# Kernel optimization log

Hardware: AMD Instinct MI355X
Metric: run time of the kernel (lower is better)

Reference implementation:

```python
import jax, jax.numpy as jnp
import numpy as np

L = 1024       # qlen
B = 2          # batch
D = 1024       # hidden_size
NH = 16        # heads
DH = 64        # d_head
NL = 4         # num_hidden_layers
MLEN = 1024    # memory length
KLEN = MLEN + L


def setup_inputs() -> dict:
    key = jax.random.key(0)
    ks = jax.random.split(key, 10)
    s = 0.02
    # causal mask: key position j is masked (True) if j > mlen + i
    attn_mask = (jnp.arange(KLEN)[None, :] > (MLEN + jnp.arange(L))[:, None])[:, :, None]
    return {
        "mems": jax.random.normal(ks[0], (NL + 1, MLEN, B, D), jnp.float32),
        "raw_embeddings": jax.random.normal(ks[1], (L, B, D), jnp.float32),
        "attention_mask": attn_mask,
        "r_w_bias": jax.random.normal(ks[2], (NH, DH), jnp.float32) * s,
        "r_r_bias": jax.random.normal(ks[3], (NH, DH), jnp.float32) * s,
        "qkv_w": jax.random.normal(ks[4], (NL, D, 3 * NH * DH), jnp.float32) * s,
        "r_w": jax.random.normal(ks[5], (NL, D, NH * DH), jnp.float32) * s,
        "o_w": jax.random.normal(ks[6], (NL, NH * DH, D), jnp.float32) * s,
        "ln1_g": jnp.ones((NL, D), jnp.float32),
        "ln1_b": jnp.zeros((NL, D), jnp.float32),
        "ff_w1": jax.random.normal(ks[7], (NL, D, D), jnp.float32) * s,
        "ff_b1": jnp.zeros((NL, D), jnp.float32),
        "ff_w2": jax.random.normal(ks[8], (NL, D, D), jnp.float32) * s,
        "ff_b2": jnp.zeros((NL, D), jnp.float32),
        "ln2_g": jnp.ones((NL, D), jnp.float32),
        "ln2_b": jnp.zeros((NL, D), jnp.float32),
    }


def _layernorm(x, g, b, eps=1e-5):
    m = jnp.mean(x, axis=-1, keepdims=True)
    v = jnp.var(x, axis=-1, keepdims=True)
    return (x - m) / jnp.sqrt(v + eps) * g + b


def _rel_shift(x):
    # x: (qlen, rlen, b, n) -> XL relative shift via pad/reshape trick
    q, r, b, n = x.shape
    xp = jnp.pad(x, ((0, 0), (1, 0), (0, 0), (0, 0)))     # (q, r+1, b, n)
    xp = xp.reshape(r + 1, q, b, n)                        # flat reinterpret
    return xp[1:].reshape(q, r, b, n)


def _forward(mems, raw_embeddings, attention_mask, r_w_bias, r_r_bias, qkv_w, r_w,
             o_w, ln1_g, ln1_b, ff_w1, ff_b1, ff_w2, ff_b2, ln2_g, ln2_b):
    qlen, bsz, d = raw_embeddings.shape
    mlen = mems.shape[1]
    klen = mlen + qlen
    nh, dh = r_w_bias.shape
    scale = 1.0 / (dh ** 0.5)

    # sinusoidal relative positional embedding: pos_seq = klen-1 ... 0
    pos_seq = jnp.arange(klen - 1, -1, -1, dtype=raw_embeddings.dtype)
    inv_freq = 1.0 / (10000.0 ** (jnp.arange(0, d, 2, dtype=jnp.float32) / d))
    sinusoid = pos_seq[:, None] * inv_freq[None, :]
    pos_emb = jnp.concatenate([jnp.sin(sinusoid), jnp.cos(sinusoid)], axis=-1)  # (klen, D)

    mask = attention_mask[:, :, :, None]  # (L, 2L, 1, 1)
    core = raw_embeddings
    hids = [core]
    n_layers = qkv_w.shape[0]
    for i in range(n_layers):
        cat = jnp.concatenate([mems[i], core], axis=0)          # (klen, b, D)
        w_heads = cat @ qkv_w[i]                                # (klen, b, 3D)
        q, k, v = jnp.split(w_heads, 3, axis=-1)
        q = q[-qlen:]
        q = q.reshape(qlen, bsz, nh, dh)
        k = k.reshape(klen, bsz, nh, dh)
        v = v.reshape(klen, bsz, nh, dh)
        r_head_k = (pos_emb @ r_w[i]).reshape(klen, nh, dh)     # (rlen, n, d)

        AC = jnp.einsum('ibnd,jbnd->ijbn', q + r_w_bias, k)
        BD = _rel_shift(jnp.einsum('ibnd,jnd->ijbn', q + r_r_bias, r_head_k))
        score = (AC + BD) * scale                               # (q, k, b, n)
        score = jnp.where(mask, -jnp.inf, score)
        prob = jax.nn.softmax(score, axis=1)
        attn_vec = jnp.einsum('ijbn,jbnd->ibnd', prob, v).reshape(qlen, bsz, nh * dh)
        attn_out = attn_vec @ o_w[i]
        core = _layernorm(core + attn_out, ln1_g[i], ln1_b[i])  # post-lnorm

        ff = jnp.maximum(core @ ff_w1[i] + ff_b1[i], 0.0) @ ff_w2[i] + ff_b2[i]
        core = _layernorm(core + ff, ln2_g[i], ln2_b[i])
        hids.append(core)

    new_mems = jax.lax.stop_gradient(jnp.stack(hids, axis=0))   # xl_grad=False -> detach
    return core, new_mems


def reference(mems, raw_embeddings, attention_mask, r_w_bias, r_r_bias, qkv_w, r_w,
              o_w, ln1_g, ln1_b, ff_w1, ff_b1, ff_w2, ff_b2, ln2_g, ln2_b):
    return _forward(mems, raw_embeddings, attention_mask, r_w_bias, r_r_bias, qkv_w,
                    r_w, o_w, ln1_g, ln1_b, ff_w1, ff_b1, ff_w2, ff_b2, ln2_g, ln2_b)
```

## Files before the change

### kernel.cpp

```cpp
#include <hip/hip_runtime.h>
#include <hip/hip_bf16.h>

#define QLEN 1024
#define BSZ 2
#define DIM 1024
#define NH 16
#define DH 64
#define NL 4
#define MLEN 1024
#define KLEN 2048
#define QROWS (QLEN*BSZ)
#define CATROWS (KLEN*BSZ)
#define N3 (3*NH*DH)

typedef __hip_bfloat16 bf16;
typedef short bf16x8_t __attribute__((ext_vector_type(8)));
typedef float f32x4_t __attribute__((ext_vector_type(4)));

__device__ __forceinline__ float b2f(bf16 h) { return __bfloat162float(h); }
__device__ __forceinline__ bf16 f2b(float f) { return __float2bfloat16(f); }
__device__ __forceinline__ short f2bs(float f) {
  bf16 h = f2b(f);
  return *reinterpret_cast<short*>(&h);
}

__device__ __forceinline__ float loadf(const void* p, size_t i, int isb) {
  return isb ? b2f(((const bf16*)p)[i]) : ((const float*)p)[i];
}
__device__ __forceinline__ void storef(void* p, size_t i, float v, int isb) {
  if (isb) ((bf16*)p)[i] = f2b(v);
  else     ((float*)p)[i] = v;
}

__device__ __forceinline__ bf16x8_t load_bf8(const bf16* p) {
  union { uint4 u; bf16x8_t v; } x;
  x.u = *reinterpret_cast<const uint4*>(p);
  return x.v;
}

__device__ __forceinline__ void gld_lds16(const bf16* g, bf16* l) {
  __builtin_amdgcn_global_load_lds(
      (const __attribute__((address_space(1))) void*)g,
      (__attribute__((address_space(3))) void*)l, 16, 0, 0);
}

__global__ void probe_kernel(const void* g, int* flag) {
  *flag = (((const unsigned int*)g)[0] == 0x3F803F80u) ? 1 : 0;
}

__global__ void pos_emb_kernel(bf16* __restrict__ pe) {
  int idx = blockIdx.x * 256 + threadIdx.x;
  int j = idx >> 10;
  int c = idx & 1023;
  int fi = (c < 512) ? c : (c - 512);
  float inv = expf(-((float)(2 * fi) * (1.0f / 1024.0f)) * 9.210340371976184f);
  float pos = (float)(KLEN - 1 - j);
  float a = pos * inv;
  float v = (c < 512) ? sinf(a) : cosf(a);
  pe[idx] = f2b(v);
}

__global__ void init_kernel(const void* __restrict__ raw, float* __restrict__ core,
                            void* __restrict__ out, const int* __restrict__ flag) {
  const int isb = *flag;
  int idx = blockIdx.x * 256 + threadIdx.x;
  float v = loadf(raw, idx, isb);
  core[idx] = v;
  storef(out, (size_t)QROWS * DIM + idx, v, isb);
}

__global__ void concat_kernel(const void* __restrict__ mems, size_t memsOff,
                              const float* __restrict__ core,
                              bf16* __restrict__ cat, const int* __restrict__ flag) {
  const int isb = *flag;
  int idx = blockIdx.x * 256 + threadIdx.x;
  const int memElems = MLEN * BSZ * DIM;
  if (idx < memElems) cat[idx] = f2b(loadf(mems, memsOff + idx, isb));
  else                cat[idx] = f2b(core[idx - memElems]);
}

__global__ void transpose5_kernel(const void* __restrict__ qkvw, const void* __restrict__ rw,
                                  const void* __restrict__ ow, const void* __restrict__ ffw1,
                                  const void* __restrict__ ffw2,
                                  bf16* __restrict__ qkvT, bf16* __restrict__ rwT,
                                  bf16* __restrict__ owT, bf16* __restrict__ f1T,
                                  bf16* __restrict__ f2T,
                                  int layer, const int* __restrict__ flag) {
  const int isb = *flag;
  __shared__ float tile[32][33];
  const int n0 = blockIdx.x * 32;
  const int k0 = blockIdx.y * 32;
  const int tx = threadIdx.x & 31;
  const int ty = threadIdx.x >> 5;
  auto doT = [&](const void* W, size_t wOff, bf16* WT, int K, int N) {
    __syncthreads();
#pragma unroll
    for (int r = 0; r < 32; r += 8)
      tile[ty + r][tx] = loadf(W, wOff + (size_t)(k0 + ty + r) * N + n0 + tx, isb);
    __syncthreads();
#pragma unroll
    for (int r = 0; r < 32; r += 8)
      WT[(size_t)(n0 + ty + r) * K + k0 + tx] = f2b(tile[tx][ty + r]);
  };
  doT(qkvw, (size_t)layer * DIM * N3, qkvT, DIM, N3);
  if (n0 < DIM) {
    const size_t o = (size_t)layer * DIM * DIM;
    doT(rw,   o, rwT, DIM, DIM);
    doT(ow,   o, owT, DIM, DIM);
    doT(ffw1, o, f1T, DIM, DIM);
    doT(ffw2, o, f2T, DIM, DIM);
  }
}

template <int EPI, int BM>
__launch_bounds__(256, 2)
__global__ void mgemm_kernel(const bf16* __restrict__ A, const bf16* __restrict__ Bt,
                             float* __restrict__ Cf, bf16* __restrict__ Ch,
                             bf16* __restrict__ Vt,
                             const void* __restrict__ bias, size_t biasOff,
                             int M, int N, int K, const int* __restrict__ flag) {
  const int isb = *flag;
  constexpr int BN = (BM == 128) ? 128 : 64;
  __shared__ bf16 As[BM * 32];
  __shared__ bf16 Bs[BN * 32];
  const int t = threadIdx.x;
  const int wave = t >> 6;
  const int lane = t & 63;
  const int g  = lane >> 4;
  const int lo = lane & 15;
  const int rowA = blockIdx.y * BM;
  const int rowB = blockIdx.x * BN;

  if constexpr (BM == 128) {
    const int wr = wave >> 1, wc = wave & 1;
    const int srow = wave * 32 + (lane >> 2);
    const int scol = (lane & 3) * 8;
    const bf16* gA = A  + (size_t)(rowA + srow) * K + scol;
    const bf16* gB = Bt + (size_t)(rowB + srow) * K + scol;
    bf16* lA = As + wave * 32 * 32;
    bf16* lB = Bs + wave * 32 * 32;

    f32x4_t acc[4][4];
#pragma unroll
    for (int m = 0; m < 4; ++m)
#pragma unroll
      for (int n = 0; n < 4; ++n) acc[m][n] = (f32x4_t){0.f, 0.f, 0.f, 0.f};

    for (int k0 = 0; k0 < K; k0 += 32) {
      gld_lds16(gA + k0, lA);
      gld_lds16(gA + (size_t)16 * K + k0, lA + 16 * 32);
      gld_lds16(gB + k0, lB);
      gld_lds16(gB + (size_t)16 * K + k0, lB + 16 * 32);
      __syncthreads();
      bf16x8_t af[4], bfr[4];
#pragma unroll
      for (int m = 0; m < 4; ++m)
        af[m] = *reinterpret_cast<const bf16x8_t*>(As + (wr * 64 + m * 16 + lo) * 32 + g * 8);
#pragma unroll
      for (int n = 0; n < 4; ++n)
        bfr[n] = *reinterpret_cast<const bf16x8_t*>(Bs + (wc * 64 + n * 16 + lo) * 32 + g * 8);
#pragma unroll
      for (int m = 0; m < 4; ++m)
#pragma unroll
        for (int n = 0; n < 4; ++n)
          acc[m][n] = __builtin_amdgcn_mfma_f32_16x16x32_bf16(af[m], bfr[n], acc[m][n], 0, 0, 0);
      __syncthreads();
    }

#pragma unroll
    for (int m = 0; m < 4; ++m) {
#pragma unroll
      for (int n = 0; n < 4; ++n) {
        const int col = rowB + wc * 64 + n * 16 + lo;
        float bv = 0.f;
        if constexpr (EPI >= 2 && EPI <= 3) bv = loadf(bias, biasOff + col, isb);
#pragma unroll
        for (int r = 0; r < 4; ++r) {
          const int row = rowA + wr * 64 + m * 16 + g * 4 + r;
          float v = acc[m][n][r];
          const size_t o = (size_t)row * N + col;
          if constexpr (EPI == 0)      Cf[o] = v;
          else if constexpr (EPI == 1) Ch[o] = f2b(v);
          else if constexpr (EPI == 2) { v += bv; Ch[o] = f2b(fmaxf(v, 0.f)); }
          else if constexpr (EPI == 3) { v += bv; Cf[o] = v; }
          else {
            if (col < 2 * DIM) Ch[o] = f2b(v);
            else Vt[((size_t)(row & 1) * DIM + (col - 2 * DIM)) * KLEN + (row >> 1)] = f2b(v);
          }
        }
      }
    }
  } else {
    const int srow = t >> 2;
    const int scol = (t & 3) * 8;
    const bf16* gA = A  + (size_t)(rowA + srow) * K + scol;
    const bf16* gB = Bt + (size_t)(rowB + srow) * K + scol;
    bf16* lA = As + wave * 16 * 32;
    bf16* lB = Bs + wave * 16 * 32;

    f32x4_t acc[4];
#pragma unroll
    for (int n = 0; n < 4; ++n) acc[n] = (f32x4_t){0.f, 0.f, 0.f, 0.f};

    for (int k0 = 0; k0 < K; k0 += 32) {
      gld_lds16(gA + k0, lA);
      gld_lds16(gB + k0, lB);
      __syncthreads();
      bf16x8_t af = *reinterpret_cast<const bf16x8_t*>(As + (wave * 16 + lo) * 32 + g * 8);
      bf16x8_t bfr[4];
#pragma unroll
      for (int n = 0; n < 4; ++n)
        bfr[n] = *reinterpret_cast<const bf16x8_t*>(Bs + (n * 16 + lo) * 32 + g * 8);
#pragma unroll
      for (int n = 0; n < 4; ++n)
        acc[n] = __builtin_amdgcn_mfma_f32_16x16x32_bf16(af, bfr[n], acc[n], 0, 0, 0);
      __syncthreads();
    }

#pragma unroll
    for (int n = 0; n < 4; ++n) {
      const int col = rowB + n * 16 + lo;
      float bv = 0.f;
      if constexpr (EPI >= 2) bv = loadf(bias, biasOff + col, isb);
#pragma unroll
      for (int r = 0; r < 4; ++r) {
        const int row = rowA + wave * 16 + g * 4 + r;
        float v = acc[n][r];
        const size_t o = (size_t)row * N + col;
        if constexpr (EPI == 0)      Cf[o] = v;
        else if constexpr (EPI == 1) Ch[o] = f2b(v);
        else if constexpr (EPI == 2) { v += bv; Ch[o] = f2b(fmaxf(v, 0.f)); }
        else if constexpr (EPI == 3) { v += bv; Cf[o] = v; }
      }
    }
  }
}

#define PSTR 56

__launch_bounds__(256, 4)
__global__ void attn_mfma_kernel(const bf16* __restrict__ wh, const bf16* __restrict__ vT,
                                 const bf16* __restrict__ rk,
                                 const void* __restrict__ rwb, const void* __restrict__ rrb,
                                 float* __restrict__ pO, float* __restrict__ pm,
                                 float* __restrict__ pl, const int* __restrict__ flag) {
  const int isb = *flag;
  const int bid = blockIdx.x;
  const int x  = bid & 7;
  const int j  = bid >> 3;
  const int head = x * 4 + (j & 3);
  const int b = head >> 4;
  const int n = head & 15;
  const int jj = j >> 2;
  const int kh = jj >> 4;
  const int s  = jj & 15;
  const int qb = (s < 8) ? s : 23 - s;
  const int qbase = qb * 64;
  const int T = 17 + qb;
  const int jstart = kh * T * 32;
  const int jlast  = jstart + (T - 1) * 32;
  const int t = threadIdx.x;
  const int wid = t >> 6;
  const int lane = t & 63;
  const int lo = lane & 15;
  const int g  = lane >> 4;
  const int i0 = qbase + wid * 16;

  __shared__ bf16 Kls[2][32 * 64];
  __shared__ bf16 Vtls[2][64 * 32];
  __shared__ bf16 Rls[128 * 64];
  __shared__ short PlsAll[4][16 * PSTR];
  short* Pl = PlsAll[wid];

  const int srow = t >> 3;
  const int kchunk = (t & 7) ^ (srow & 7);
  const size_t rowStride = (size_t)BSZ * N3;
  const bf16* gK  = wh + ((size_t)srow * BSZ + b) * N3 + DIM + n * DH + kchunk * 8;
  const bf16* gVt = vT + ((size_t)b * DIM + n * DH + (t >> 2)) * KLEN
                       + (((t & 3) ^ ((t >> 3) & 3)) << 3);

  auto stageR = [&](int s0) {
    int r = s0 + (t >> 3);
    int rc = (r < KLEN) ? r : (KLEN - 1);
    const bf16* src = rk + (size_t)rc * DIM + n * DH + ((t & 7) ^ ((t >> 3) & 7)) * 8;
    gld_lds16(src, &Rls[(size_t)(s0 & 127) * 64 + (size_t)wid * 512]);
  };

  bf16x8_t qw[2], qr[2];
  {
    const bf16* qrow = wh + ((size_t)(MLEN + i0 + lo) * BSZ + b) * N3 + n * DH;
#pragma unroll
    for (int c = 0; c < 2; ++c) {
      int d0 = c * 32 + g * 8;
#pragma unroll
      for (int jj2 = 0; jj2 < 8; ++jj2) {
        float qv = b2f(qrow[d0 + jj2]);
        qw[c][jj2] = f2bs(qv + loadf(rwb, n * DH + d0 + jj2, isb));
        qr[c][jj2] = f2bs(qv + loadf(rrb, n * DH + d0 + jj2, isb));
      }
    }
  }

  f32x4_t O[4];
  float mrow[4], lrow[4];
#pragma unroll
  for (int d = 0; d < 4; ++d) { O[d] = (f32x4_t){0.f, 0.f, 0.f, 0.f}; }
#pragma unroll
  for (int r = 0; r < 4; ++r) { mrow[r] = -INFINITY; lrow[r] = 0.f; }

  const float SCL = 0.125f * 1.44269504088896f;

  gld_lds16(gK + (size_t)jstart * rowStride, &Kls[0][wid * 512]);
  gld_lds16(gVt + jstart, &Vtls[0][wid * 512]);
  stageR(MLEN - 64 - qbase + jstart);
  stageR(MLEN - 32 - qbase + jstart);
  stageR(MLEN - qbase + jstart);
  __syncthreads();

  int bi = 0;
  for (int j0 = jstart; j0 <= jlast; j0 += 32) {
    if (j0 < jlast) {
      gld_lds16(gK + (size_t)(j0 + 32) * rowStride, &Kls[bi ^ 1][wid * 512]);
      gld_lds16(gVt + j0 + 32, &Vtls[bi ^ 1][wid * 512]);
      stageR(MLEN + 32 + j0 - qbase);
    }
    const bf16* Kl  = Kls[bi];
    const bf16* Vtl = Vtls[bi];

    f32x4_t s2[2];
    s2[0] = (f32x4_t){0.f, 0.f, 0.f, 0.f};
    s2[1] = (f32x4_t){0.f, 0.f, 0.f, 0.f};
#pragma unroll
    for (int c = 0; c < 2; ++c) {
#pragma unroll
      for (int tt = 0; tt < 2; ++tt) {
        const int row = tt * 16 + lo;
        const bf16* kp = Kl + row * 64 + (((c * 4 + g) ^ (row & 7)) << 3);
        s2[tt] = __builtin_amdgcn_mfma_f32_16x16x32_bf16(qw[c], load_bf8(kp), s2[tt], 0, 0, 0);
      }
    }
    const int u0 = MLEN - 1 + j0 - i0 - 15;
    f32x4_t dacc[3];
    dacc[0] = (f32x4_t){0.f, 0.f, 0.f, 0.f};
    dacc[1] = (f32x4_t){0.f, 0.f, 0.f, 0.f};
    dacc[2] = (f32x4_t){0.f, 0.f, 0.f, 0.f};
#pragma unroll
    for (int c = 0; c < 2; ++c) {
#pragma unroll
      for (int tt = 0; tt < 3; ++tt) {
        const int sr = (u0 + tt * 16 + lo) & 127;
        const bf16* rp = Rls + sr * 64 + (((c * 4 + g) ^ (lo & 7)) << 3);
        dacc[tt] = __builtin_amdgcn_mfma_f32_16x16x32_bf16(qr[c], load_bf8(rp), dacc[tt], 0, 0, 0);
      }
    }

    float sv[2][4];
#pragma unroll
    for (int r = 0; r < 4; ++r) {
      const int ri = g * 4 + r;
      const int srcl = g * 16 + ((lo + 15 - ri) & 15);
      float a0 = __shfl(dacc[0][r], srcl);
      float a1 = __shfl(dacc[1][r], srcl);
      float a2 = __shfl(dacc[2][r], srcl);
      const bool hi = lo > ri;
      float d0 = hi ? a1 : a0;
      float d1 = hi ? a2 : a1;
      bool v0 = (kh == 0) || ((j0 + lo)      <= (MLEN + i0 + ri));
      bool v1 = (kh == 0) || ((j0 + lo + 16) <= (MLEN + i0 + ri));
      sv[0][r] = v0 ? (s2[0][r] + d0) * SCL : -INFINITY;
      sv[1][r] = v1 ? (s2[1][r] + d1) * SCL : -INFINITY;
    }

    float alpha[4];
#pragma unroll
    for (int r = 0; r < 4; ++r) {
      float v = fmaxf(sv[0][r], sv[1][r]);
      v = fmaxf(v, __shfl_xor(v, 1));
      v = fmaxf(v, __shfl_xor(v, 2));
      v = fmaxf(v, __shfl_xor(v, 4));
      v = fmaxf(v, __shfl_xor(v, 8));
      float mn = fmaxf(mrow[r], v);
      alpha[r] = exp2f(mrow[r] - mn);
      mrow[r] = mn;
    }
    float ps[2][4];
#pragma unroll
    for (int f2 = 0; f2 < 2; ++f2)
#pragma unroll
      for (int r = 0; r < 4; ++r)
        ps[f2][r] = exp2f(sv[f2][r] - mrow[r]);
#pragma unroll
    for (int r = 0; r < 4; ++r) {
      float v = ps[0][r] + ps[1][r];
      v += __shfl_xor(v, 1);
      v += __shfl_xor(v, 2);
      v += __shfl_xor(v, 4);
      v += __shfl_xor(v, 8);
      lrow[r] = lrow[r] * alpha[r] + v;
    }
#pragma unroll
    for (int d = 0; d < 4; ++d)
#pragma unroll
      for (int r = 0; r < 4; ++r)
        O[d][r] *= alpha[r];

#pragma unroll
    for (int f2 = 0; f2 < 2; ++f2)
#pragma unroll
      for (int r = 0; r < 4; ++r)
        Pl[(g * 4 + r) * PSTR + lo + 16 * f2] = f2bs(ps[f2][r]);
    __builtin_amdgcn_wave_barrier();
    bf16x8_t pf = *reinterpret_cast<const bf16x8_t*>(&Pl[lo * PSTR + g * 8]);

#pragma unroll
    for (int dt = 0; dt < 4; ++dt) {
      const int vrow = dt * 16 + lo;
      bf16x8_t vf = load_bf8(Vtl + vrow * 32 + ((g ^ ((lo >> 1) & 3)) << 3));
      O[dt] = __builtin_amdgcn_mfma_f32_16x16x32_bf16(pf, vf, O[dt], 0, 0, 0);
    }

    __syncthreads();
    bi ^= 1;
  }

#pragma unroll
  for (int dt = 0; dt < 4; ++dt)
#pragma unroll
    for (int r = 0; r < 4; ++r) {
      const int ri = g * 4 + r;
      pO[((size_t)kh * QROWS + (size_t)(i0 + ri) * BSZ + b) * DIM
         + n * DH + dt * 16 + lo] = O[dt][r];
    }
  if (lo == 0) {
#pragma unroll
    for (int r = 0; r < 4; ++r) {
      const int ri = g * 4 + r;
      const size_t sidx = (((size_t)kh * BSZ + b) * NH + n) * QLEN + (i0 + ri);
      pm[sidx] = mrow[r];
      pl[sidx] = lrow[r];
    }
  }
}

__launch_bounds__(256)
__global__ void attn_merge_kernel(const float* __restrict__ pO, const float* __restrict__ pm,
                                  const float* __restrict__ pl, bf16* __restrict__ av) {
  const int row = blockIdx.x;
  const int i = row >> 1;
  const int b = row & 1;
  const int t = threadIdx.x;
  const size_t SH = (size_t)BSZ * NH * QLEN;
#pragma unroll
  for (int u = 0; u < 4; ++u) {
    const int d = t + u * 256;
    const int n = d >> 6;
    const size_t sidx = ((size_t)b * NH + n) * QLEN + i;
    const float m0 = pm[sidx], m1 = pm[SH + sidx];
    const float l0 = pl[sidx], l1 = pl[SH + sidx];
    const float m = fmaxf(m0, m1);
    const float c0 = exp2f(m0 - m), c1 = exp2f(m1 - m);
    const float O0 = pO[(size_t)row * DIM + d];
    const float O1 = pO[((size_t)QROWS + row) * DIM + d];
    av[(size_t)row * DIM + d] = f2b((O0 * c0 + O1 * c1) / (l0 * c0 + l1 * c1));
  }
}

template <bool WRITE_HID>
__launch_bounds__(256)
__global__ void resid_ln_kernel(const float* __restrict__ base, const float* __restrict__ add,
                                const void* __restrict__ g, size_t gOff,
                                const void* __restrict__ bta, size_t btaOff,
                                float* __restrict__ core_f, bf16* __restrict__ core_h,
                                void* __restrict__ out, size_t hidOff,
                                const int* __restrict__ flag) {
  const int isb = *flag;
  const int row = blockIdx.x;
  const int t = threadIdx.x;
  __shared__ float red[256];
  __shared__ float red2[256];
  float x[4];
  float s = 0.f, sq = 0.f;
#pragma unroll
  for (int u = 0; u < 4; ++u) {
    int idx = t + u * 256;
    float v = base[(size_t)row * DIM + idx] + add[(size_t)row * DIM + idx];
    x[u] = v; s += v; sq += v * v;
  }
  red[t] = s; red2[t] = sq; __syncthreads();
#pragma unroll
  for (int s2 = 128; s2 > 0; s2 >>= 1) {
    if (t < s2) { red[t] += red[t + s2]; red2[t] += red2[t + s2]; }
    __syncthreads();
  }
  const float mean = red[0] * (1.0f / DIM);
  const float var  = red2[0] * (1.0f / DIM) - mean * mean;
  const float rstd = rsqrtf(var + 1e-5f);
#pragma unroll
  for (int u = 0; u < 4; ++u) {
    int idx = t + u * 256;
    float y = (x[u] - mean) * rstd * loadf(g, gOff + idx, isb) + loadf(bta, btaOff + idx, isb);
    core_f[(size_t)row * DIM + idx] = y;
    core_h[(size_t)row * DIM + idx] = f2b(y);
    if (WRITE_HID) storef(out, hidOff + (size_t)row * DIM + idx, y, isb);
  }
}

__global__ void copy_out_kernel(const float* __restrict__ src, void* __restrict__ out,
                                const int* __restrict__ flag) {
  const int isb = *flag;
  int idx = blockIdx.x * 256 + threadIdx.x;
  storef(out, idx, src[idx], isb);
}

extern "C" void kernel_launch(void* const* d_in, const int* in_sizes, int n_in,
                              void* d_out, int out_size, void* d_ws, size_t ws_size,
                              hipStream_t stream) {
  const void* mems = d_in[0];
  const void* raw  = d_in[1];
  const void* rwb  = d_in[3];
  const void* rrb  = d_in[4];
  const void* qkvw = d_in[5];
  const void* rw   = d_in[6];
  const void* ow   = d_in[7];
  const void* ln1g = d_in[8];
  const void* ln1b = d_in[9];
  const void* ffw1 = d_in[10];
  const void* ffb1 = d_in[11];
  const void* ffw2 = d_in[12];
  const void* ffb2 = d_in[13];
  const void* ln2g = d_in[14];
  const void* ln2b = d_in[15];

  char* w = (char*)d_ws;
  size_t off = 0;
  auto alloc = [&](size_t bytes) -> void* {
    void* p = w + off;
    off += (bytes + 255) & ~(size_t)255;
    return p;
  };
  int*   flag    = (int*)alloc(4);
  bf16*  pos_emb = (bf16*)alloc((size_t)KLEN * DIM * 2);
  bf16*  wh      = (bf16*)alloc((size_t)CATROWS * N3 * 2);
  bf16*  cat     = (bf16*)alloc((size_t)CATROWS * DIM * 2);
  bf16*  rk      = (bf16*)alloc((size_t)KLEN * DIM * 2);
  float* core_f  = (float*)alloc((size_t)QROWS * DIM * 4);
  bf16*  vT      = (bf16*)alloc((size_t)2 * DIM * KLEN * 2);
  float* pO      = (float*)alloc((size_t)2 * QROWS * DIM * 4);
  float* pm      = (float*)alloc((size_t)2 * BSZ * NH * QLEN * 4);
  float* pl      = (float*)alloc((size_t)2 * BSZ * NH * QLEN * 4);
  bf16*  qkvT    = (bf16*)alloc((size_t)N3 * DIM * 2);
  bf16*  rwT     = (bf16*)alloc((size_t)DIM * DIM * 2);
  bf16*  owT     = (bf16*)alloc((size_t)DIM * DIM * 2);
  bf16*  f1T     = (bf16*)alloc((size_t)DIM * DIM * 2);
  bf16*  f2T     = (bf16*)alloc((size_t)DIM * DIM * 2);
  float* buf1   = (float*)wh;
  bf16*  buf2   = (bf16*)((char*)wh + (size_t)8 * 1024 * 1024);
  bf16*  avec   = cat;
  bf16*  core_h = (bf16*)((char*)cat + (size_t)4 * 1024 * 1024);
  (void)ws_size; (void)in_sizes; (void)n_in; (void)out_size;

  const size_t HID = (size_t)QROWS * DIM;

  probe_kernel<<<1, 1, 0, stream>>>(ln1g, flag);
  pos_emb_kernel<<<KLEN * DIM / 256, 256, 0, stream>>>(pos_emb);
  init_kernel<<<QROWS * DIM / 256, 256, 0, stream>>>(raw, core_f, d_out, flag);

  for (int i = 0; i < NL; ++i) {
    const size_t memsOff = (size_t)i * MLEN * BSZ * DIM;
    transpose5_kernel<<<dim3(96, 32), 256, 0, stream>>>(
        qkvw, rw, ow, ffw1, ffw2, qkvT, rwT, owT, f1T, f2T, i, flag);
    concat_kernel<<<CATROWS * DIM / 256, 256, 0, stream>>>(mems, memsOff, core_f, cat, flag);
    mgemm_kernel<4, 128><<<dim3(N3 / 128, CATROWS / 128), 256, 0, stream>>>(
        cat, qkvT, nullptr, wh, vT, nullptr, 0, CATROWS, N3, DIM, flag);
    mgemm_kernel<1, 64><<<dim3(DIM / 64, KLEN / 64), 256, 0, stream>>>(
        pos_emb, rwT, nullptr, rk, nullptr, nullptr, 0, KLEN, DIM, DIM, flag);
    attn_mfma_kernel<<<1024, 256, 0, stream>>>(wh, vT, rk, rwb, rrb, pO, pm, pl, flag);
    attn_merge_kernel<<<QROWS, 256, 0, stream>>>(pO, pm, pl, avec);
    mgemm_kernel<0, 64><<<dim3(DIM / 64, QROWS / 64), 256, 0, stream>>>(
        avec, owT, buf1, nullptr, nullptr, nullptr, 0, QROWS, DIM, DIM, flag);
    resid_ln_kernel<false><<<QROWS, 256, 0, stream>>>(
        core_f, buf1, ln1g, (size_t)i * DIM, ln1b, (size_t)i * DIM,
        core_f, core_h, nullptr, 0, flag);
    mgemm_kernel<2, 64><<<dim3(DIM / 64, QROWS / 64), 256, 0, stream>>>(
        core_h, f1T, nullptr, buf2, nullptr, ffb1, (size_t)i * DIM, QROWS, DIM, DIM, flag);
    mgemm_kernel<3, 64><<<dim3(DIM / 64, QROWS / 64), 256, 0, stream>>>(
        buf2, f2T, buf1, nullptr, nullptr, ffb2, (size_t)i * DIM, QROWS, DIM, DIM, flag);
    resid_ln_kernel<true><<<QROWS, 256, 0, stream>>>(
        core_f, buf1, ln2g, (size_t)i * DIM, ln2b, (size_t)i * DIM,
        core_f, core_h, d_out, HID * (size_t)(i + 2), flag);
  }
  copy_out_kernel<<<QROWS * DIM / 256, 256, 0, stream>>>(core_f, d_out, flag);
}
```

Measured before the change: 1.248 ms.

## Double-buffer 64-tile GEMM with K=64 stages and XOR swizzle; vectorize attn merge

Splits the 64x64 GEMM path into a separate kernel that loads K=64 slices into double-buffered LDS. The next tile is prefetched while the current one is computed, and an XOR swizzle avoids LDS bank conflicts. This halves the number of barriers per K step and hides global-load latency. The attention merge kernel now has each thread handle four contiguous elements, using float4 loads, one reciprocal and a packed bf16 store. The cost is more LDS per block (32KB), which may reduce occupancy, and relies on load_bf8 existing in the hidden code.

```diff
diff --git a/kernel.cpp b/kernel.cpp
--- a/kernel.cpp
+++ b/kernel.cpp
@@ -112,7 +112,7 @@
   }
 }
 
-template <int EPI, int BM>
+template <int EPI>
 __launch_bounds__(256, 2)
 __global__ void mgemm_kernel(const bf16* __restrict__ A, const bf16* __restrict__ Bt,
                              float* __restrict__ Cf, bf16* __restrict__ Ch,
@@ -120,118 +120,144 @@
                              const void* __restrict__ bias, size_t biasOff,
                              int M, int N, int K, const int* __restrict__ flag) {
   const int isb = *flag;
-  constexpr int BN = (BM == 128) ? 128 : 64;
-  __shared__ bf16 As[BM * 32];
-  __shared__ bf16 Bs[BN * 32];
+  __shared__ bf16 As[128 * 32];
+  __shared__ bf16 Bs[128 * 32];
   const int t = threadIdx.x;
   const int wave = t >> 6;
   const int lane = t & 63;
   const int g  = lane >> 4;
   const int lo = lane & 15;
-  const int rowA = blockIdx.y * BM;
-  const int rowB = blockIdx.x * BN;
-
-  if constexpr (BM == 128) {
-    const int wr = wave >> 1, wc = wave & 1;
-    const int srow = wave * 32 + (lane >> 2);
-    const int scol = (lane & 3) * 8;
-    const bf16* gA = A  + (size_t)(rowA + srow) * K + scol;
-    const bf16* gB = Bt + (size_t)(rowB + srow) * K + scol;
-    bf16* lA = As + wave * 32 * 32;
-    bf16* lB = Bs + wave * 32 * 32;
-
-    f32x4_t acc[4][4];
+  const int wr = wave >> 1, wc = wave & 1;
+  const int rowA = blockIdx.y * 128;
+  const int rowB = blockIdx.x * 128;
+
+  const int srow = wave * 32 + (lane >> 2);
+  const int scol = (lane & 3) * 8;
+  const bf16* gA = A  + (size_t)(rowA + srow) * K + scol;
+  const bf16* gB = Bt + (size_t)(rowB + srow) * K + scol;
+  bf16* lA = As + wave * 32 * 32;
+  bf16* lB = Bs + wave * 32 * 32;
+
+  f32x4_t acc[4][4];
+#pragma unroll
+  for (int m = 0; m < 4; ++m)
+#pragma unroll
+    for (int n = 0; n < 4; ++n) acc[m][n] = (f32x4_t){0.f, 0.f, 0.f, 0.f};
+
+  for (int k0 = 0; k0 < K; k0 += 32) {
+    gld_lds16(gA + k0, lA);
+    gld_lds16(gA + (size_t)16 * K + k0, lA + 16 * 32);
+    gld_lds16(gB + k0, lB);
+    gld_lds16(gB + (size_t)16 * K + k0, lB + 16 * 32);
+    __syncthreads();
+    bf16x8_t af[4], bfr[4];
 #pragma unroll
     for (int m = 0; m < 4; ++m)
-#pragma unroll
-      for (int n = 0; n < 4; ++n) acc[m][n] = (f32x4_t){0.f, 0.f, 0.f, 0.f};
-
-    for (int k0 = 0; k0 < K; k0 += 32) {
-      gld_lds16(gA + k0, lA);
-      gld_lds16(gA + (size_t)16 * K + k0, lA + 16 * 32);
-      gld_lds16(gB + k0, lB);
-      gld_lds16(gB + (size_t)16 * K + k0, lB + 16 * 32);
-      __syncthreads();
-      bf16x8_t af[4], bfr[4];
-#pragma unroll
-      for (int m = 0; m < 4; ++m)
-        af[m] = *reinterpret_cast<const bf16x8_t*>(As + (wr * 64 + m * 16 + lo) * 32 + g * 8);
+      af[m] = *reinterpret_cast<const bf16x8_t*>(As + (wr * 64 + m * 16 + lo) * 32 + g * 8);
+#pragma unroll
+    for (int n = 0; n < 4; ++n)
+      bfr[n] = *reinterpret_cast<const bf16x8_t*>(Bs + (wc * 64 + n * 16 + lo) * 32 + g * 8);
+#pragma unroll
+    for (int m = 0; m < 4; ++m)
 #pragma unroll
       for (int n = 0; n < 4; ++n)
-        bfr[n] = *reinterpret_cast<const bf16x8_t*>(Bs + (wc * 64 + n * 16 + lo) * 32 + g * 8);
-#pragma unroll
-      for (int m = 0; m < 4; ++m)
-#pragma unroll
-        for (int n = 0; n < 4; ++n)
-          acc[m][n] = __builtin_amdgcn_mfma_f32_16x16x32_bf16(af[m], bfr[n], acc[m][n], 0, 0, 0);
-      __syncthreads();
-    }
-
-#pragma unroll
-    for (int m = 0; m < 4; ++m) {
-#pragma unroll
-      for (int n = 0; n < 4; ++n) {
-        const int col = rowB + wc * 64 + n * 16 + lo;
-        float bv = 0.f;
-        if constexpr (EPI >= 2 && EPI <= 3) bv = loadf(bias, biasOff + col, isb);
-#pragma unroll
-        for (int r = 0; r < 4; ++r) {
-          const int row = rowA + wr * 64 + m * 16 + g * 4 + r;
-          float v = acc[m][n][r];
-          const size_t o = (size_t)row * N + col;
-          if constexpr (EPI == 0)      Cf[o] = v;
-          else if constexpr (EPI == 1) Ch[o] = f2b(v);
-          else if constexpr (EPI == 2) { v += bv; Ch[o] = f2b(fmaxf(v, 0.f)); }
-          else if constexpr (EPI == 3) { v += bv; Cf[o] = v; }
-          else {
-            if (col < 2 * DIM) Ch[o] = f2b(v);
-            else Vt[((size_t)(row & 1) * DIM + (col - 2 * DIM)) * KLEN + (row >> 1)] = f2b(v);
-          }
-        }
-      }
-    }
-  } else {
-    const int srow = t >> 2;
-    const int scol = (t & 3) * 8;
-    const bf16* gA = A  + (size_t)(rowA + srow) * K + scol;
-    const bf16* gB = Bt + (size_t)(rowB + srow) * K + scol;
-    bf16* lA = As + wave * 16 * 32;
-    bf16* lB = Bs + wave * 16 * 32;
-
-    f32x4_t acc[4];
-#pragma unroll
-    for (int n = 0; n < 4; ++n) acc[n] = (f32x4_t){0.f, 0.f, 0.f, 0.f};
-
-    for (int k0 = 0; k0 < K; k0 += 32) {
-      gld_lds16(gA + k0, lA);
-      gld_lds16(gB + k0, lB);
-      __syncthreads();
-      bf16x8_t af = *reinterpret_cast<const bf16x8_t*>(As + (wave * 16 + lo) * 32 + g * 8);
-      bf16x8_t bfr[4];
-#pragma unroll
-      for (int n = 0; n < 4; ++n)
-        bfr[n] = *reinterpret_cast<const bf16x8_t*>(Bs + (n * 16 + lo) * 32 + g * 8);
-#pragma unroll
-      for (int n = 0; n < 4; ++n)
-        acc[n] = __builtin_amdgcn_mfma_f32_16x16x32_bf16(af, bfr[n], acc[n], 0, 0, 0);
-      __syncthreads();
-    }
-
+        acc[m][n] = __builtin_amdgcn_mfma_f32_16x16x32_bf16(af[m], bfr[n], acc[m][n], 0, 0, 0);
+    __syncthreads();
+  }
+
+#pragma unroll
+  for (int m = 0; m < 4; ++m) {
 #pragma unroll
     for (int n = 0; n < 4; ++n) {
-      const int col = rowB + n * 16 + lo;
+      const int col = rowB + wc * 64 + n * 16 + lo;
       float bv = 0.f;
-      if constexpr (EPI >= 2) bv = loadf(bias, biasOff + col, isb);
+      if constexpr (EPI >= 2 && EPI <= 3) bv = loadf(bias, biasOff + col, isb);
 #pragma unroll
       for (int r = 0; r < 4; ++r) {
-        const int row = rowA + wave * 16 + g * 4 + r;
-        float v = acc[n][r];
+        const int row = rowA + wr * 64 + m * 16 + g * 4 + r;
+        float v = acc[m][n][r];
         const size_t o = (size_t)row * N + col;
         if constexpr (EPI == 0)      Cf[o] = v;
         else if constexpr (EPI == 1) Ch[o] = f2b(v);
         else if constexpr (EPI == 2) { v += bv; Ch[o] = f2b(fmaxf(v, 0.f)); }
         else if constexpr (EPI == 3) { v += bv; Cf[o] = v; }
+        else {
+          if (col < 2 * DIM) Ch[o] = f2b(v);
+          else Vt[((size_t)(row & 1) * DIM + (col - 2 * DIM)) * KLEN + (row >> 1)] = f2b(v);
+        }
       }
+    }
+  }
+}
+
+template <int EPI>
+__launch_bounds__(256, 2)
+__global__ void mgemm64_kernel(const bf16* __restrict__ A, const bf16* __restrict__ Bt,
+                               float* __restrict__ Cf, bf16* __restrict__ Ch,
+                               const void* __restrict__ bias, size_t biasOff,
+                               int M, int N, int K, const int* __restrict__ flag) {
+  const int isb = *flag;
+  __shared__ bf16 As[2][64 * 64];
+  __shared__ bf16 Bs[2][64 * 64];
+  const int t = threadIdx.x;
+  const int wave = t >> 6;
+  const int lane = t & 63;
+  const int g  = lane >> 4;
+  const int lo = lane & 15;
+  const int rowA = blockIdx.y * 64;
+  const int rowB = blockIdx.x * 64;
+
+  const int sr  = wave * 16 + (lane >> 3);
+  const int sch = (lane & 7) ^ ((lane >> 3) & 7);
+  const bf16* gA = A  + (size_t)(rowA + sr) * K + sch * 8;
+  const bf16* gB = Bt + (size_t)(rowB + sr) * K + sch * 8;
+
+  f32x4_t acc[4];
+#pragma unroll
+  for (int n = 0; n < 4; ++n) acc[n] = (f32x4_t){0.f, 0.f, 0.f, 0.f};
+
+  auto stage = [&](int buf, int k0) {
+    gld_lds16(gA + k0,                 &As[buf][wave * 1024]);
+    gld_lds16(gA + (size_t)8 * K + k0, &As[buf][wave * 1024 + 512]);
+    gld_lds16(gB + k0,                 &Bs[buf][wave * 1024]);
+    gld_lds16(gB + (size_t)8 * K + k0, &Bs[buf][wave * 1024 + 512]);
+  };
+
+  stage(0, 0);
+  __syncthreads();
+  int bi = 0;
+  const int nst = K >> 6;
+  for (int ks = 0; ks < nst; ++ks) {
+    if (ks + 1 < nst) stage(bi ^ 1, (ks + 1) << 6);
+    bf16x8_t af[2];
+#pragma unroll
+    for (int c = 0; c < 2; ++c)
+      af[c] = load_bf8(&As[bi][(wave * 16 + lo) * 64 + (((c * 4 + g) ^ (lo & 7)) << 3)]);
+#pragma unroll
+    for (int c = 0; c < 2; ++c)
+#pragma unroll
+      for (int n = 0; n < 4; ++n) {
+        bf16x8_t bf = load_bf8(&Bs[bi][(n * 16 + lo) * 64 + (((c * 4 + g) ^ (lo & 7)) << 3)]);
+        acc[n] = __builtin_amdgcn_mfma_f32_16x16x32_bf16(af[c], bf, acc[n], 0, 0, 0);
+      }
+    __syncthreads();
+    bi ^= 1;
+  }
+
+#pragma unroll
+  for (int n = 0; n < 4; ++n) {
+    const int col = rowB + n * 16 + lo;
+    float bv = 0.f;
+    if constexpr (EPI >= 2) bv = loadf(bias, biasOff + col, isb);
+#pragma unroll
+    for (int r = 0; r < 4; ++r) {
+      const int row = rowA + wave * 16 + g * 4 + r;
+      float v = acc[n][r];
+      const size_t o = (size_t)row * N + col;
+      if constexpr (EPI == 0)      Cf[o] = v;
+      else if constexpr (EPI == 1) Ch[o] = f2b(v);
+      else if constexpr (EPI == 2) { v += bv; Ch[o] = f2b(fmaxf(v, 0.f)); }
+      else                         { v += bv; Cf[o] = v; }
     }
   }
 }
@@ -448,21 +474,23 @@
   const int row = blockIdx.x;
   const int i = row >> 1;
   const int b = row & 1;
-  const int t = threadIdx.x;
+  const int d0 = threadIdx.x * 4;
+  const int n = d0 >> 6;
   const size_t SH = (size_t)BSZ * NH * QLEN;
-#pragma unroll
-  for (int u = 0; u < 4; ++u) {
-    const int d = t + u * 256;
-    const int n = d >> 6;
-    const size_t sidx = ((size_t)b * NH + n) * QLEN + i;
-    const float m0 = pm[sidx], m1 = pm[SH + sidx];
-    const float l0 = pl[sidx], l1 = pl[SH + sidx];
-    const float m = fmaxf(m0, m1);
-    const float c0 = exp2f(m0 - m), c1 = exp2f(m1 - m);
-    const float O0 = pO[(size_t)row * DIM + d];
-    const float O1 = pO[((size_t)QROWS + row) * DIM + d];
-    av[(size_t)row * DIM + d] = f2b((O0 * c0 + O1 * c1) / (l0 * c0 + l1 * c1));
-  }
+  const size_t sidx = ((size_t)b * NH + n) * QLEN + i;
+  const float m0 = pm[sidx], m1 = pm[SH + sidx];
+  const float l0 = pl[sidx], l1 = pl[SH + sidx];
+  const float m = fmaxf(m0, m1);
+  const float c0 = exp2f(m0 - m), c1 = exp2f(m1 - m);
+  const float inv = 1.0f / (l0 * c0 + l1 * c1);
+  const float4 O0 = *reinterpret_cast<const float4*>(&pO[(size_t)row * DIM + d0]);
+  const float4 O1 = *reinterpret_cast<const float4*>(&pO[((size_t)QROWS + row) * DIM + d0]);
+  union { short s[4]; uint2 u; } o;
+  o.s[0] = f2bs((O0.x * c0 + O1.x * c1) * inv);
+  o.s[1] = f2bs((O0.y * c0 + O1.y * c1) * inv);
+  o.s[2] = f2bs((O0.z * c0 + O1.z * c1) * inv);
+  o.s[3] = f2bs((O0.w * c0 + O1.w * c1) * inv);
+  *reinterpret_cast<uint2*>(&av[(size_t)row * DIM + d0]) = o.u;
 }
 
 template <bool WRITE_HID>
@@ -570,21 +598,21 @@
     transpose5_kernel<<<dim3(96, 32), 256, 0, stream>>>(
         qkvw, rw, ow, ffw1, ffw2, qkvT, rwT, owT, f1T, f2T, i, flag);
     concat_kernel<<<CATROWS * DIM / 256, 256, 0, stream>>>(mems, memsOff, core_f, cat, flag);
-    mgemm_kernel<4, 128><<<dim3(N3 / 128, CATROWS / 128), 256, 0, stream>>>(
+    mgemm_kernel<4><<<dim3(N3 / 128, CATROWS / 128), 256, 0, stream>>>(
         cat, qkvT, nullptr, wh, vT, nullptr, 0, CATROWS, N3, DIM, flag);
-    mgemm_kernel<1, 64><<<dim3(DIM / 64, KLEN / 64), 256, 0, stream>>>(
-        pos_emb, rwT, nullptr, rk, nullptr, nullptr, 0, KLEN, DIM, DIM, flag);
+    mgemm64_kernel<1><<<dim3(DIM / 64, KLEN / 64), 256, 0, stream>>>(
+        pos_emb, rwT, nullptr, rk, nullptr, 0, KLEN, DIM, DIM, flag);
     attn_mfma_kernel<<<1024, 256, 0, stream>>>(wh, vT, rk, rwb, rrb, pO, pm, pl, flag);
     attn_merge_kernel<<<QROWS, 256, 0, stream>>>(pO, pm, pl, avec);
-    mgemm_kernel<0, 64><<<dim3(DIM / 64, QROWS / 64), 256, 0, stream>>>(
-        avec, owT, buf1, nullptr, nullptr, nullptr, 0, QROWS, DIM, DIM, flag);
+    mgemm64_kernel<0><<<dim3(DIM / 64, QROWS / 64), 256, 0, stream>>>(
+        avec, owT, buf1, nullptr, nullptr, 0, QROWS, DIM, DIM, flag);
     resid_ln_kernel<false><<<QROWS, 256, 0, stream>>>(
         core_f, buf1, ln1g, (size_t)i * DIM, ln1b, (size_t)i * DIM,
         core_f, core_h, nullptr, 0, flag);
-    mgemm_kernel<2, 64><<<dim3(DIM / 64, QROWS / 64), 256, 0, stream>>>(
-        core_h, f1T, nullptr, buf2, nullptr, ffb1, (size_t)i * DIM, QROWS, DIM, DIM, flag);
-    mgemm_kernel<3, 64><<<dim3(DIM / 64, QROWS / 64), 256, 0, stream>>>(
-        buf2, f2T, buf1, nullptr, nullptr, ffb2, (size_t)i * DIM, QROWS, DIM, DIM, flag);
+    mgemm64_kernel<2><<<dim3(DIM / 64, QROWS / 64), 256, 0, stream>>>(
+        core_h, f1T, nullptr, buf2, ffb1, (size_t)i * DIM, QROWS, DIM, DIM, flag);
+    mgemm64_kernel<3><<<dim3(DIM / 64, QROWS / 64), 256, 0, stream>>>(
+        buf2, f2T, buf1, nullptr, ffb2, (size_t)i * DIM, QROWS, DIM, DIM, flag);
     resid_ln_kernel<true><<<QROWS, 256, 0, stream>>>(
         core_f, buf1, ln2g, (size_t)i * DIM, ln2b, (size_t)i * DIM,
         core_f, core_h, d_out, HID * (size_t)(i + 2), flag);
```

After: 1.140 ms. 1.09x faster.
